# Kernel tuning notes

Measured on AMD Instinct MI355X. Metric: run time of the kernel, lower is better.

## Reference

```python
import jax, jax.numpy as jnp
import numpy as np

N = 50000
E = 800000
IN = 128
HEADS = 4
C = 32  # out_features per head
HC = HEADS * C


def setup_inputs() -> dict:
    key = jax.random.key(0)
    ks = jax.random.split(key, 10)
    s_in = 1.0 / np.sqrt(IN)
    x = jax.random.normal(ks[0], (N, IN), dtype=jnp.float32)
    edge_index = jax.random.randint(ks[1], (2, E), 0, N, dtype=jnp.int64)
    Wq = jax.random.normal(ks[2], (IN, HC), dtype=jnp.float32) * s_in
    bq = jnp.zeros((HC,), dtype=jnp.float32)
    Wk = jax.random.normal(ks[3], (IN, HC), dtype=jnp.float32) * s_in
    bk = jnp.zeros((HC,), dtype=jnp.float32)
    Wv = jax.random.normal(ks[4], (IN, HC), dtype=jnp.float32) * s_in
    bv = jnp.zeros((HC,), dtype=jnp.float32)
    Wskip = jax.random.normal(ks[5], (IN, HC), dtype=jnp.float32) * s_in
    bskip = jnp.zeros((HC,), dtype=jnp.float32)
    return {"x": x, "edge_index": edge_index, "Wq": Wq, "bq": bq,
            "Wk": Wk, "bk": bk, "Wv": Wv, "bv": bv,
            "Wskip": Wskip, "bskip": bskip}


def reference(x, edge_index, Wq, bq, Wk, bk, Wv, bv, Wskip, bskip):
    src = edge_index[0]  # message source j
    dst = edge_index[1]  # message target i

    q = (x @ Wq + bq).reshape(N, HEADS, C)
    k = (x @ Wk + bk).reshape(N, HEADS, C)
    v = (x @ Wv + bv).reshape(N, HEADS, C)

    # per-edge attention logits: [E, H]
    logits = jnp.einsum('ehc,ehc->eh', q[dst], k[src]) / jnp.sqrt(
        jnp.asarray(C, dtype=x.dtype))

    # segment softmax over incoming edges of each target node
    seg_max = jax.ops.segment_max(logits, dst, num_segments=N)
    seg_max = jnp.where(jnp.isfinite(seg_max), seg_max, 0.0)
    expd = jnp.exp(logits - seg_max[dst])
    seg_sum = jax.ops.segment_sum(expd, dst, num_segments=N)
    alpha = expd / (seg_sum[dst] + 1e-16)  # [E, H]

    # scatter-add weighted values: [N, H, C]
    msgs = alpha[:, :, None] * v[src]
    out = jax.ops.segment_sum(msgs, dst, num_segments=N)
    out = out.reshape(N, HC) + (x @ Wskip + bskip)  # root/skip connection

    # LeakyReLU(negative_slope=0.2)
    return jnp.where(out >= 0, out, 0.2 * out)
```

## Files before the change

### kernel.cpp

```cpp
#include <hip/hip_runtime.h>

#define N_NODES 50000
#define E_EDGES 800000
#define IN_F 128
#define HC 128
#define ROWTILES 3125
#define PACK_BLOCKS 32
#define HIST_BLOCKS 3125
#define CAP 64

typedef __attribute__((ext_vector_type(8))) short short8;
typedef __attribute__((ext_vector_type(4))) float floatx4;

__device__ __forceinline__ unsigned short f2bf(float f) {
    union { float f; unsigned u; } x; x.f = f;
    unsigned r = x.u + 0x7FFF + ((x.u >> 16) & 1);
    return (unsigned short)(r >> 16);
}
__device__ __forceinline__ float bflo(unsigned u) {
    union { unsigned u; float f; } c; c.u = u << 16; return c.f;
}
__device__ __forceinline__ float bfhi(unsigned u) {
    union { unsigned u; float f; } c; c.u = u & 0xFFFF0000u; return c.f;
}
__device__ __forceinline__ int swzb(int b) { return b ^ (((b >> 10) & 3) << 5); }
__device__ __forceinline__ int swzf(int b) { return b ^ (((b >> 11) & 3) << 5); }

__global__ __launch_bounds__(256) void pack_w(
    const float* __restrict__ Wq, const float* __restrict__ Wk,
    const float* __restrict__ Wv, const float* __restrict__ Ws,
    const float* __restrict__ bq, const float* __restrict__ bk,
    const float* __restrict__ bv, const float* __restrict__ bs,
    short* __restrict__ bpack, float* __restrict__ bcat,
    int* __restrict__ cnt)
{
    int t = blockIdx.x * 256 + threadIdx.x;
    int lane = t & 63, ks = (t >> 6) & 3, nt = t >> 8;
    int col = nt * 16 + (lane & 15);
    int sec = col >> 7, c = col & 127;
    const float* W = sec == 0 ? Wq : sec == 1 ? Wk : sec == 2 ? Wv : Ws;
    int kbase = ks * 32 + (lane >> 4) * 8;
    short8 b;
#pragma unroll
    for (int j = 0; j < 8; j++) b[j] = (short)f2bf(W[(size_t)(kbase + j) * HC + c]);
    *(short8*)(bpack + (size_t)t * 8) = b;
    if (t < 512) {
        int s2 = t >> 7, c2 = t & 127;
        bcat[t] = (s2 == 0 ? bq : s2 == 1 ? bk : s2 == 2 ? bv : bs)[c2];
    }
    for (int i = t; i < N_NODES; i += PACK_BLOCKS * 256) cnt[i] = 0;
}

__global__ __launch_bounds__(256) void gemm_hist(
    const float* __restrict__ x, const short* __restrict__ bpack,
    const float* __restrict__ bcat,
    unsigned short* __restrict__ q, unsigned short* __restrict__ k,
    unsigned short* __restrict__ v, float* __restrict__ out,
    const int* __restrict__ src, const int* __restrict__ dst,
    int* __restrict__ cnt, int* __restrict__ ssrc)
{
    if (blockIdx.x >= ROWTILES) {
        int e = (blockIdx.x - ROWTILES) * 256 + threadIdx.x;
        int d = dst[e];
        int r = atomicAdd(&cnt[d], 1);
        if (r < CAP) ssrc[(size_t)d * CAP + r] = src[e];
        return;
    }
    __shared__ __align__(16) unsigned char lds[3 * 4096 + 8192];

    const int rt = blockIdx.x;
    const int cg = threadIdx.x >> 6;
    const int lane = threadIdx.x & 63;
    const int l16 = lane & 15, kh = lane >> 4;

    short8 a[4];
    const size_t row = (size_t)rt * 16 + l16;
#pragma unroll
    for (int ks = 0; ks < 4; ks++) {
        const float* p0 = x + row * IN_F + ks * 32 + kh * 8;
        float4 lo = *(const float4*)p0;
        float4 hi = *(const float4*)(p0 + 4);
        short8 aa;
        aa[0] = (short)f2bf(lo.x); aa[1] = (short)f2bf(lo.y);
        aa[2] = (short)f2bf(lo.z); aa[3] = (short)f2bf(lo.w);
        aa[4] = (short)f2bf(hi.x); aa[5] = (short)f2bf(hi.y);
        aa[6] = (short)f2bf(hi.z); aa[7] = (short)f2bf(hi.w);
        a[ks] = aa;
    }

    unsigned char* Eb = lds + cg * 4096;
    unsigned char* Ef = lds + 12288;

#pragma unroll
    for (int nt8 = 0; nt8 < 8; nt8++) {
        const int nt = cg * 8 + nt8;
        floatx4 acc = {0.f, 0.f, 0.f, 0.f};
#pragma unroll
        for (int ks = 0; ks < 4; ks++) {
            short8 b = *(const short8*)(bpack + ((size_t)(nt * 4 + ks) * 64 + lane) * 8);
            acc = __builtin_amdgcn_mfma_f32_16x16x32_bf16(a[ks], b, acc, 0, 0, 0);
        }
        const float bias = bcat[cg * 128 + nt8 * 16 + l16];
        if (cg < 3) {
#pragma unroll
            for (int r = 0; r < 4; r++) {
                int boff = ((kh * 4 + r) * 128 + nt8 * 16 + l16) * 2;
                *(unsigned short*)(Eb + swzb(boff)) = f2bf(acc[r] + bias);
            }
        } else {
#pragma unroll
            for (int r = 0; r < 4; r++) {
                int boff = ((kh * 4 + r) * 128 + nt8 * 16 + l16) * 4;
                *(float*)(Ef + swzf(boff)) = acc[r] + bias;
            }
        }
    }

    if (cg < 3) {
        unsigned short* gout = ((cg == 0) ? q : (cg == 1) ? k : v)
                               + (size_t)rt * 16 * HC;
#pragma unroll
        for (int i = 0; i < 4; i++) {
            int idx = i * 64 + lane;
            uint4 val = *(const uint4*)(Eb + swzb(idx * 16));
            *(uint4*)(gout + idx * 8) = val;
        }
    } else {
        float* gout = out + (size_t)rt * 16 * HC;
#pragma unroll
        for (int i = 0; i < 8; i++) {
            int idx = i * 64 + lane;
            float4 val = *(const float4*)(Ef + swzf(idx * 16));
            *(float4*)(gout + idx * 4) = val;
        }
    }
}

__global__ __launch_bounds__(256) void node_attn(
    const unsigned short* __restrict__ q, const unsigned short* __restrict__ k,
    const unsigned short* __restrict__ v, const int* __restrict__ cnt,
    const int* __restrict__ ssrc, float* __restrict__ out)
{
    const int wave = (blockIdx.x * 256 + threadIdx.x) >> 6;
    if (wave >= N_NODES) return;
    const int lane = threadIdx.x & 63;
    const int node = wave;

    union { unsigned u; float f; } cv;
    const unsigned uq = *(const unsigned*)(q + (size_t)node * HC + lane * 2);
    cv.u = uq << 16;          float qx = cv.f;
    cv.u = uq & 0xFFFF0000u;  float qy = cv.f;

    float accx = 0.f, accy = 0.f, ssum = 0.f;
    int deg = __builtin_amdgcn_readfirstlane(cnt[node]);
    if (deg > CAP) deg = CAP;
    const int* sp = ssrc + (size_t)node * CAP;
    const float scale = 0.17677669529663687f;

    int e = 0;
    for (; e + 3 < deg; e += 4) {
        const int j0 = sp[e],     j1 = sp[e + 1];
        const int j2 = sp[e + 2], j3 = sp[e + 3];
        const unsigned uk0 = *(const unsigned*)(k + (size_t)j0 * HC + lane * 2);
        const unsigned uk1 = *(const unsigned*)(k + (size_t)j1 * HC + lane * 2);
        const unsigned uk2 = *(const unsigned*)(k + (size_t)j2 * HC + lane * 2);
        const unsigned uk3 = *(const unsigned*)(k + (size_t)j3 * HC + lane * 2);
        const unsigned uv0 = *(const unsigned*)(v + (size_t)j0 * HC + lane * 2);
        const unsigned uv1 = *(const unsigned*)(v + (size_t)j1 * HC + lane * 2);
        const unsigned uv2 = *(const unsigned*)(v + (size_t)j2 * HC + lane * 2);
        const unsigned uv3 = *(const unsigned*)(v + (size_t)j3 * HC + lane * 2);
        float p0, p1, p2, p3;
        { float kx, ky;
          cv.u = uk0 << 16; kx = cv.f; cv.u = uk0 & 0xFFFF0000u; ky = cv.f;
          p0 = qx * kx + qy * ky;
          cv.u = uk1 << 16; kx = cv.f; cv.u = uk1 & 0xFFFF0000u; ky = cv.f;
          p1 = qx * kx + qy * ky;
          cv.u = uk2 << 16; kx = cv.f; cv.u = uk2 & 0xFFFF0000u; ky = cv.f;
          p2 = qx * kx + qy * ky;
          cv.u = uk3 << 16; kx = cv.f; cv.u = uk3 & 0xFFFF0000u; ky = cv.f;
          p3 = qx * kx + qy * ky; }
#pragma unroll
        for (int off = 1; off <= 8; off <<= 1) {
            p0 += __shfl_xor(p0, off);
            p1 += __shfl_xor(p1, off);
            p2 += __shfl_xor(p2, off);
            p3 += __shfl_xor(p3, off);
        }
        const float w0 = __expf(p0 * scale);
        const float w1 = __expf(p1 * scale);
        const float w2 = __expf(p2 * scale);
        const float w3 = __expf(p3 * scale);
        { float vx, vy;
          cv.u = uv0 << 16; vx = cv.f; cv.u = uv0 & 0xFFFF0000u; vy = cv.f;
          accx += w0 * vx; accy += w0 * vy;
          cv.u = uv1 << 16; vx = cv.f; cv.u = uv1 & 0xFFFF0000u; vy = cv.f;
          accx += w1 * vx; accy += w1 * vy;
          cv.u = uv2 << 16; vx = cv.f; cv.u = uv2 & 0xFFFF0000u; vy = cv.f;
          accx += w2 * vx; accy += w2 * vy;
          cv.u = uv3 << 16; vx = cv.f; cv.u = uv3 & 0xFFFF0000u; vy = cv.f;
          accx += w3 * vx; accy += w3 * vy; }
        ssum += (w0 + w1) + (w2 + w3);
    }
    for (; e < deg; e++) {
        const int j0 = sp[e];
        const unsigned uk0 = *(const unsigned*)(k + (size_t)j0 * HC + lane * 2);
        const unsigned uv0 = *(const unsigned*)(v + (size_t)j0 * HC + lane * 2);
        float kx, ky;
        cv.u = uk0 << 16; kx = cv.f; cv.u = uk0 & 0xFFFF0000u; ky = cv.f;
        float p0 = qx * kx + qy * ky;
        p0 += __shfl_xor(p0, 1);
        p0 += __shfl_xor(p0, 2);
        p0 += __shfl_xor(p0, 4);
        p0 += __shfl_xor(p0, 8);
        const float w0 = __expf(p0 * scale);
        float vx, vy;
        cv.u = uv0 << 16; vx = cv.f; cv.u = uv0 & 0xFFFF0000u; vy = cv.f;
        accx += w0 * vx; accy += w0 * vy;
        ssum += w0;
    }

    const float inv = 1.0f / (ssum + 1e-16f);
    const float2 sk = *(const float2*)(out + (size_t)node * HC + lane * 2);
    float ox = accx * inv + sk.x;
    float oy = accy * inv + sk.y;
    ox = ox >= 0.f ? ox : 0.2f * ox;
    oy = oy >= 0.f ? oy : 0.2f * oy;
    *(float2*)(out + (size_t)node * HC + lane * 2) = make_float2(ox, oy);
}

extern "C" void kernel_launch(void* const* d_in, const int* in_sizes, int n_in,
                              void* d_out, int out_size, void* d_ws, size_t ws_size,
                              hipStream_t stream)
{
    const float* x    = (const float*)d_in[0];
    const int*   ei   = (const int*)d_in[1];
    const float* Wq   = (const float*)d_in[2];
    const float* bq   = (const float*)d_in[3];
    const float* Wk   = (const float*)d_in[4];
    const float* bk   = (const float*)d_in[5];
    const float* Wv   = (const float*)d_in[6];
    const float* bv   = (const float*)d_in[7];
    const float* Wsk  = (const float*)d_in[8];
    const float* bsk  = (const float*)d_in[9];
    float* out = (float*)d_out;

    char* w = (char*)d_ws;
    const size_t NFB = (size_t)N_NODES * HC * sizeof(unsigned short);
    unsigned short* q = (unsigned short*)w;            w += NFB;
    unsigned short* k = (unsigned short*)w;            w += NFB;
    unsigned short* v = (unsigned short*)w;            w += NFB;
    short* bpack = (short*)w;                          w += 8192 * 8 * sizeof(short);
    float* bcat  = (float*)w;                          w += 512 * sizeof(float);
    int* cnt  = (int*)w;                               w += N_NODES * sizeof(int);
    int* ssrc = (int*)w;

    const int* srcIdx = ei;
    const int* dstIdx = ei + E_EDGES;

    pack_w<<<PACK_BLOCKS, 256, 0, stream>>>(Wq, Wk, Wv, Wsk, bq, bk, bv, bsk,
                                            bpack, bcat, cnt);
    gemm_hist<<<ROWTILES + HIST_BLOCKS, 256, 0, stream>>>(
        x, bpack, bcat, q, k, v, out, srcIdx, dstIdx, cnt, ssrc);
    node_attn<<<(N_NODES * 64) / 256, 256, 0, stream>>>(q, k, v, cnt, ssrc, out);
}
```

Baseline: 157.5 us.

## Split histogram from GEMM and process two row tiles per GEMM block

Moves the edge histogram/bucketing out of the fused GEMM launch into its own kernel with 512-thread blocks. The GEMM kernel now computes two 16-row tiles per block, reusing each loaded weight fragment for both tiles, and prefetches the next weight fragment while the current MFMAs run. This is meant to halve weight reloads and improve MFMA issue density. In exchange it adds a separate launch, serialises the histogram before the GEMM, and doubles LDS per block, which may reduce occupancy.

```diff
diff --git a/kernel.cpp b/kernel.cpp
--- a/kernel.cpp
+++ b/kernel.cpp
@@ -6,7 +6,7 @@
 #define HC 128
 #define ROWTILES 3125
 #define PACK_BLOCKS 32
-#define HIST_BLOCKS 3125
+#define GEMM_BLOCKS 1563
 #define CAP 64
 
 typedef __attribute__((ext_vector_type(8))) short short8;
@@ -51,87 +51,128 @@
     for (int i = t; i < N_NODES; i += PACK_BLOCKS * 256) cnt[i] = 0;
 }
 
-__global__ __launch_bounds__(256) void gemm_hist(
+__global__ __launch_bounds__(512) void hist_k(
+    const int* __restrict__ src, const int* __restrict__ dst,
+    int* __restrict__ cnt, int* __restrict__ ssrc)
+{
+    int e = blockIdx.x * 512 + threadIdx.x;
+    if (e < E_EDGES) {
+        int d = dst[e];
+        int r = atomicAdd(&cnt[d], 1);
+        if (r < CAP) ssrc[(size_t)d * CAP + r] = src[e];
+    }
+}
+
+__global__ __launch_bounds__(256) void gemm_k(
     const float* __restrict__ x, const short* __restrict__ bpack,
     const float* __restrict__ bcat,
     unsigned short* __restrict__ q, unsigned short* __restrict__ k,
-    unsigned short* __restrict__ v, float* __restrict__ out,
-    const int* __restrict__ src, const int* __restrict__ dst,
-    int* __restrict__ cnt, int* __restrict__ ssrc)
-{
-    if (blockIdx.x >= ROWTILES) {
-        int e = (blockIdx.x - ROWTILES) * 256 + threadIdx.x;
-        int d = dst[e];
-        int r = atomicAdd(&cnt[d], 1);
-        if (r < CAP) ssrc[(size_t)d * CAP + r] = src[e];
-        return;
-    }
-    __shared__ __align__(16) unsigned char lds[3 * 4096 + 8192];
-
-    const int rt = blockIdx.x;
+    unsigned short* __restrict__ v, float* __restrict__ out)
+{
+    __shared__ __align__(16) unsigned char lds[2 * 20480];
+
     const int cg = threadIdx.x >> 6;
     const int lane = threadIdx.x & 63;
     const int l16 = lane & 15, kh = lane >> 4;
-
-    short8 a[4];
-    const size_t row = (size_t)rt * 16 + l16;
-#pragma unroll
-    for (int ks = 0; ks < 4; ks++) {
-        const float* p0 = x + row * IN_F + ks * 32 + kh * 8;
-        float4 lo = *(const float4*)p0;
-        float4 hi = *(const float4*)(p0 + 4);
-        short8 aa;
-        aa[0] = (short)f2bf(lo.x); aa[1] = (short)f2bf(lo.y);
-        aa[2] = (short)f2bf(lo.z); aa[3] = (short)f2bf(lo.w);
-        aa[4] = (short)f2bf(hi.x); aa[5] = (short)f2bf(hi.y);
-        aa[6] = (short)f2bf(hi.z); aa[7] = (short)f2bf(hi.w);
-        a[ks] = aa;
-    }
-
-    unsigned char* Eb = lds + cg * 4096;
-    unsigned char* Ef = lds + 12288;
-
-#pragma unroll
+    const int rt0 = blockIdx.x * 2;
+    const bool has1 = (rt0 + 1) < ROWTILES;
+
+    short8 a[2][4];
+#pragma unroll
+    for (int t = 0; t < 2; t++) {
+        const size_t row = (size_t)(t && has1 ? rt0 + 1 : rt0) * 16 + l16;
+#pragma unroll
+        for (int ks = 0; ks < 4; ks++) {
+            const float* p0 = x + row * IN_F + ks * 32 + kh * 8;
+            float4 lo = *(const float4*)p0;
+            float4 hi = *(const float4*)(p0 + 4);
+            short8 aa;
+            aa[0] = (short)f2bf(lo.x); aa[1] = (short)f2bf(lo.y);
+            aa[2] = (short)f2bf(lo.z); aa[3] = (short)f2bf(lo.w);
+            aa[4] = (short)f2bf(hi.x); aa[5] = (short)f2bf(hi.y);
+            aa[6] = (short)f2bf(hi.z); aa[7] = (short)f2bf(hi.w);
+            a[t][ks] = aa;
+        }
+    }
+
+    float bias[8];
+#pragma unroll
+    for (int n = 0; n < 8; n++) bias[n] = bcat[cg * 128 + n * 16 + l16];
+
+    unsigned char* E0b = lds + cg * 4096;
+    unsigned char* E1b = lds + 20480 + cg * 4096;
+    unsigned char* E0f = lds + 12288;
+    unsigned char* E1f = lds + 20480 + 12288;
+
+    const int ntb = cg * 8;
+    short8 bc[4], bn[4];
+#pragma unroll
+    for (int ks = 0; ks < 4; ks++)
+        bc[ks] = *(const short8*)(bpack + ((size_t)(ntb * 4 + ks) * 64 + lane) * 8);
+
+#pragma unroll 1
     for (int nt8 = 0; nt8 < 8; nt8++) {
-        const int nt = cg * 8 + nt8;
-        floatx4 acc = {0.f, 0.f, 0.f, 0.f};
+        if (nt8 < 7) {
+#pragma unroll
+            for (int ks = 0; ks < 4; ks++)
+                bn[ks] = *(const short8*)(bpack + ((size_t)((ntb + nt8 + 1) * 4 + ks) * 64 + lane) * 8);
+        }
+        floatx4 acc0 = {0.f, 0.f, 0.f, 0.f}, acc1 = {0.f, 0.f, 0.f, 0.f};
 #pragma unroll
         for (int ks = 0; ks < 4; ks++) {
-            short8 b = *(const short8*)(bpack + ((size_t)(nt * 4 + ks) * 64 + lane) * 8);
-            acc = __builtin_amdgcn_mfma_f32_16x16x32_bf16(a[ks], b, acc, 0, 0, 0);
-        }
-        const float bias = bcat[cg * 128 + nt8 * 16 + l16];
+            acc0 = __builtin_amdgcn_mfma_f32_16x16x32_bf16(a[0][ks], bc[ks], acc0, 0, 0, 0);
+            acc1 = __builtin_amdgcn_mfma_f32_16x16x32_bf16(a[1][ks], bc[ks], acc1, 0, 0, 0);
+        }
+        const float bs_ = bias[nt8];
         if (cg < 3) {
 #pragma unroll
             for (int r = 0; r < 4; r++) {
                 int boff = ((kh * 4 + r) * 128 + nt8 * 16 + l16) * 2;
-                *(unsigned short*)(Eb + swzb(boff)) = f2bf(acc[r] + bias);
+                *(unsigned short*)(E0b + swzb(boff)) = f2bf(acc0[r] + bs_);
+                *(unsigned short*)(E1b + swzb(boff)) = f2bf(acc1[r] + bs_);
             }
         } else {
 #pragma unroll
             for (int r = 0; r < 4; r++) {
                 int boff = ((kh * 4 + r) * 128 + nt8 * 16 + l16) * 4;
-                *(float*)(Ef + swzf(boff)) = acc[r] + bias;
+                *(float*)(E0f + swzf(boff)) = acc0[r] + bs_;
+                *(float*)(E1f + swzf(boff)) = acc1[r] + bs_;
             }
         }
+#pragma unroll
+        for (int ks = 0; ks < 4; ks++) bc[ks] = bn[ks];
     }
 
     if (cg < 3) {
-        unsigned short* gout = ((cg == 0) ? q : (cg == 1) ? k : v)
-                               + (size_t)rt * 16 * HC;
+        unsigned short* base = (cg == 0) ? q : (cg == 1) ? k : v;
+        unsigned short* g0 = base + (size_t)rt0 * 16 * HC;
 #pragma unroll
         for (int i = 0; i < 4; i++) {
             int idx = i * 64 + lane;
-            uint4 val = *(const uint4*)(Eb + swzb(idx * 16));
-            *(uint4*)(gout + idx * 8) = val;
+            *(uint4*)(g0 + idx * 8) = *(const uint4*)(E0b + swzb(idx * 16));
+        }
+        if (has1) {
+            unsigned short* g1 = base + (size_t)(rt0 + 1) * 16 * HC;
+#pragma unroll
+            for (int i = 0; i < 4; i++) {
+                int idx = i * 64 + lane;
+                *(uint4*)(g1 + idx * 8) = *(const uint4*)(E1b + swzb(idx * 16));
+            }
         }
     } else {
-        float* gout = out + (size_t)rt * 16 * HC;
+        float* g0 = out + (size_t)rt0 * 16 * HC;
 #pragma unroll
         for (int i = 0; i < 8; i++) {
             int idx = i * 64 + lane;
-            float4 val = *(const float4*)(Ef + swzf(idx * 16));
-            *(float4*)(gout + idx * 4) = val;
+            *(float4*)(g0 + idx * 4) = *(const float4*)(E0f + swzf(idx * 16));
+        }
+        if (has1) {
+            float* g1 = out + (size_t)(rt0 + 1) * 16 * HC;
+#pragma unroll
+            for (int i = 0; i < 8; i++) {
+                int idx = i * 64 + lane;
+                *(float4*)(g1 + idx * 4) = *(const float4*)(E1f + swzf(idx * 16));
+            }
         }
     }
 }
@@ -259,7 +300,8 @@
 
     pack_w<<<PACK_BLOCKS, 256, 0, stream>>>(Wq, Wk, Wv, Wsk, bq, bk, bv, bsk,
                                             bpack, bcat, cnt);
-    gemm_hist<<<ROWTILES + HIST_BLOCKS, 256, 0, stream>>>(
-        x, bpack, bcat, q, k, v, out, srcIdx, dstIdx, cnt, ssrc);
+    hist_k<<<(E_EDGES + 511) / 512, 512, 0, stream>>>(srcIdx, dstIdx, cnt, ssrc);
+    gemm_k<<<GEMM_BLOCKS, 256, 0, stream>>>(
+        x, bpack, bcat, q, k, v, out);
     node_attn<<<(N_NODES * 64) / 256, 256, 0, stream>>>(q, k, v, cnt, ssrc, out);
 }
```

Result: faster. 148.2 us (-5.9%).
